# Performance work log

Hardware: AMD Instinct MI355X
Metric: run time of the kernel (lower is better)

## Reference

```python
import jax, jax.numpy as jnp
import numpy as np

NUM_HIGH = 3  # init arg num_high


def conv_gauss(img, kernel):
    # reflect pad 2 on H/W, then 5x5 depthwise conv (groups = C)
    img = jnp.pad(img, ((0, 0), (0, 0), (2, 2), (2, 2)), mode='reflect')
    C = img.shape[1]
    return jax.lax.conv_general_dilated(
        img, kernel, window_strides=(1, 1), padding='VALID',
        dimension_numbers=('NCHW', 'OIHW', 'NCHW'), feature_group_count=C)


def upsample(x, kernel):
    # zero-interleave in H and W (equivalent to the cat/view/permute chain),
    # then gaussian depthwise conv
    B, C, H, W = x.shape
    up = jnp.zeros((B, C, 2 * H, 2 * W), dtype=x.dtype).at[:, :, ::2, ::2].set(x)
    return conv_gauss(up, kernel)


def setup_inputs() -> dict:
    key = jax.random.key(0)
    k1, k2 = jax.random.split(key)
    img = jax.random.normal(k1, (16, 3, 512, 512), dtype=jnp.float32)
    kernel = jax.random.normal(k2, (3, 1, 5, 5), dtype=jnp.float32) * 0.04
    return {"img": img, "kernel": kernel}


def reference(img, kernel):
    # pyramid_decom: with even H/W at every level, up always matches current's
    # shape, so the bicubic-interpolate fallback branch is dead (as in torch).
    current = img
    pyr = []
    for _ in range(NUM_HIGH):
        filtered = conv_gauss(current, kernel)
        down = filtered[:, :, ::2, ::2]
        up = upsample(down, kernel)
        pyr.append(current - up)
        current = down
    pyr.append(current)
    return tuple(pyr)
```

## Files before the change

### kernel.cpp

```cpp
#include <hip/hip_runtime.h>


#define B_ 16
#define C_ 3
#define DX 64
#define EW 72
#define SDW 72

typedef float f4v __attribute__((ext_vector_type(4)));
typedef float f2v __attribute__((ext_vector_type(2)));

__device__ __forceinline__ int reflect101(int t, int n) {
    t = (t < 0) ? -t : t;
    return (t >= n) ? (2 * n - 2 - t) : t;
}

template<int LOG2HW, int DY, bool NTST>
__global__ __launch_bounds__(32 * DY, 8) void lap_level_t(
    const float* __restrict__ in, const float* __restrict__ kern,
    float* __restrict__ down, float* __restrict__ pyr)
{
    constexpr int H  = 1 << LOG2HW, W = H;
    constexpr int H2 = H >> 1,      W2 = W >> 1;
    constexpr int IH = 2 * DY + 7;

    __shared__ float sE[IH][EW];
    __shared__ float sO[IH][EW];
    __shared__ float sDn[DY + 2][SDW];

    const int bc  = blockIdx.z;
    const int c   = bc % C_;
    const int dx0 = blockIdx.x * DX;
    const int dy0 = blockIdx.y * DY;
    const int gx0 = 2 * dx0 - 4;
    const int gy0 = 2 * dy0 - 4;
    const int tid = threadIdx.x;

    float kk[25];
    {
        const float* kc = kern + c * 25;
        #pragma unroll
        for (int i = 0; i < 25; ++i) kk[i] = kc[i];
    }

    const float* src = in + (size_t)bc * H * W;

    {
        const int q  = tid & 31;
        const int gx = gx0 + 4 * q;
        const bool colOK = (gx >= 0) && (gx + 3 < W);
        const int rb = tid >> 5;
        const float* p0 = src + (size_t)reflect101(gy0 + rb,      H) * W;
        const float* p1 = src + (size_t)reflect101(gy0 + rb + DY, H) * W;
        const float* p2 = src + (size_t)reflect101(gy0 + ((rb + 2 * DY < IH) ? rb + 2 * DY : rb), H) * W;
        float4 v0, v1, v2;
        if (colOK) {
            v0 = *(const float4*)(p0 + gx);
            v1 = *(const float4*)(p1 + gx);
            v2 = *(const float4*)(p2 + gx);
        } else {
            const int c0 = reflect101(gx, W), c1 = reflect101(gx + 1, W),
                      c2 = reflect101(gx + 2, W), c3 = reflect101(gx + 3, W);
            v0 = make_float4(p0[c0], p0[c1], p0[c2], p0[c3]);
            v1 = make_float4(p1[c0], p1[c1], p1[c2], p1[c3]);
            v2 = make_float4(p2[c0], p2[c1], p2[c2], p2[c3]);
        }
        *(float2*)&sE[rb][2 * q]      = make_float2(v0.x, v0.z);
        *(float2*)&sO[rb][2 * q]      = make_float2(v0.y, v0.w);
        *(float2*)&sE[rb + DY][2 * q] = make_float2(v1.x, v1.z);
        *(float2*)&sO[rb + DY][2 * q] = make_float2(v1.y, v1.w);
        if (rb + 2 * DY < IH) {
            *(float2*)&sE[rb + 2 * DY][2 * q] = make_float2(v2.x, v2.z);
            *(float2*)&sO[rb + 2 * DY][2 * q] = make_float2(v2.y, v2.w);
        }
        if (tid < 4 * IH && (tid & 3) < 3) {
            const int r   = tid >> 2;
            const int q2  = 32 + (tid & 3);
            const int gx2 = gx0 + 4 * q2;
            const float* row = src + (size_t)reflect101(gy0 + r, H) * W;
            float4 v;
            if (gx2 >= 0 && gx2 + 3 < W) v = *(const float4*)(row + gx2);
            else v = make_float4(row[reflect101(gx2, W)], row[reflect101(gx2 + 1, W)],
                                 row[reflect101(gx2 + 2, W)], row[reflect101(gx2 + 3, W)]);
            *(float2*)&sE[r][2 * q2] = make_float2(v.x, v.z);
            *(float2*)&sO[r][2 * q2] = make_float2(v.y, v.w);
        }
    }
    __syncthreads();

    {
        constexpr int NDM = (DY + 2) * 16;
        if (tid < NDM + (DY + 2)) {
            int dr, m0;
            if (tid < NDM) { dr = tid >> 4; m0 = (tid & 15) << 2; }
            else           { dr = tid - NDM; m0 = 64; }
            float o0 = 0.f, o1 = 0.f, o2 = 0.f, o3 = 0.f;
            #pragma unroll
            for (int i = 0; i < 5; ++i) {
                const int r = 2 * dr + i;
                const float4 e0 = *(const float4*)&sE[r][m0];
                const float2 e1 = *(const float2*)&sE[r][m0 + 4];
                const float4 q0 = *(const float4*)&sO[r][m0];
                const float2 q1 = *(const float2*)&sO[r][m0 + 4];
                const float k0 = kk[5*i], k1 = kk[5*i+1], k2 = kk[5*i+2],
                            k3 = kk[5*i+3], k4 = kk[5*i+4];
                o0 += e0.x * k0 + q0.x * k1 + e0.y * k2 + q0.y * k3 + e0.z * k4;
                o1 += e0.y * k0 + q0.y * k1 + e0.z * k2 + q0.z * k3 + e0.w * k4;
                o2 += e0.z * k0 + q0.z * k1 + e0.w * k2 + q0.w * k3 + e1.x * k4;
                o3 += e0.w * k0 + q0.w * k1 + e1.x * k2 + q1.x * k3 + e1.y * k4;
            }
            *(f4v*)&sDn[dr][m0] = (f4v){o0, o1, o2, o3};
        }
    }
    __syncthreads();

    {
        const int pq  = tid & 31;
        const int pr  = tid >> 5;
        const int gdy = dy0 + pr;
        const int rows0 = (gdy == 0)      ? pr + 2 : pr;
        const int rows1 = pr + 1;
        const int rows2 = (gdy == H2 - 1) ? pr + 1 : pr + 2;
        const bool leftE  = (dx0 == 0 && pq == 0);
        const bool rightE = (dx0 + 2 * pq + 1 == W2 - 1);

        float uee_a = 0, ueo_a = 0, uoe_a = 0, uoo_a = 0;
        float uee_b = 0, ueo_b = 0, uoe_b = 0, uoo_b = 0;
        #pragma unroll
        for (int i = 0; i < 3; ++i) {
            const int rr = (i == 0) ? rows0 : (i == 1) ? rows1 : rows2;
            const float2 va = *(const float2*)&sDn[rr][2 * pq];
            const float2 vb = *(const float2*)&sDn[rr][2 * pq + 2];
            float aL = va.x, aC = va.y, aR = vb.x;
            float bL = va.y, bC = vb.x, bR = vb.y;
            if (leftE)  aL = aR;
            if (rightE) bR = bC;
            uee_a += aL * kk[10*i+0] + aC * kk[10*i+2] + aR * kk[10*i+4];
            ueo_a += aC * kk[10*i+1] + aR * kk[10*i+3];
            uee_b += bL * kk[10*i+0] + bC * kk[10*i+2] + bR * kk[10*i+4];
            ueo_b += bC * kk[10*i+1] + bR * kk[10*i+3];
            if (i) {
                uoe_a += aL * kk[10*i-5] + aC * kk[10*i-3] + aR * kk[10*i-1];
                uoo_a += aC * kk[10*i-4] + aR * kk[10*i-2];
                uoe_b += bL * kk[10*i-5] + bC * kk[10*i-3] + bR * kk[10*i-1];
                uoo_b += bC * kk[10*i-4] + bR * kk[10*i-2];
            }
            if (i == 1) {
                float* dp = down + (size_t)bc * H2 * W2 + (size_t)gdy * W2 + dx0 + 2 * pq;
                if constexpr (NTST) __builtin_nontemporal_store((f2v){aC, bC}, (f2v*)dp);
                else                *(float2*)dp = make_float2(aC, bC);
            }
        }

        const int ly = 2 * pr + 4;
        const int u  = 2 * pq + 2;
        const float2 e0 = *(const float2*)&sE[ly][u];
        const float2 q0 = *(const float2*)&sO[ly][u];
        const float2 e1 = *(const float2*)&sE[ly + 1][u];
        const float2 q1 = *(const float2*)&sO[ly + 1][u];

        float* py = pyr + (size_t)bc * H * W;
        const size_t base = (size_t)(2 * gdy) * W + (2 * dx0 + 4 * pq);
        const f4v o0 = {e0.x - uee_a, q0.x - ueo_a, e0.y - uee_b, q0.y - ueo_b};
        const f4v o1 = {e1.x - uoe_a, q1.x - uoo_a, e1.y - uoe_b, q1.y - uoo_b};
        __builtin_nontemporal_store(o0, (f4v*)(py + base));
        __builtin_nontemporal_store(o1, (f4v*)(py + base + W));
    }
}

__global__ __launch_bounds__(256) void down_kernel(
    const float* __restrict__ in, const float* __restrict__ kern,
    float* __restrict__ out, int H, int W)
{
    const int H2 = H >> 1, W2 = W >> 1;
    const int bc = blockIdx.z;
    const int c  = bc % C_;
    __shared__ float k[25];
    int tid = threadIdx.y * blockDim.x + threadIdx.x;
    if (tid < 25) k[tid] = kern[c * 25 + tid];
    __syncthreads();
    int x = blockIdx.x * blockDim.x + threadIdx.x;
    int y = blockIdx.y * blockDim.y + threadIdx.y;
    if (x >= W2 || y >= H2) return;
    const float* img = in + (size_t)bc * H * W;
    const int bx = 2 * x - 2, by = 2 * y - 2;
    float acc = 0.f;
    if (bx >= 0 && by >= 0 && bx + 4 < W && by + 4 < H) {
        const float* p = img + (size_t)by * W + bx;
        #pragma unroll
        for (int dy = 0; dy < 5; ++dy) {
            #pragma unroll
            for (int dx = 0; dx < 5; ++dx) acc += p[dx] * k[dy * 5 + dx];
            p += W;
        }
    } else {
        #pragma unroll
        for (int dy = 0; dy < 5; ++dy) {
            const float* row = img + (size_t)reflect101(by + dy, H) * W;
            #pragma unroll
            for (int dx = 0; dx < 5; ++dx) acc += row[reflect101(bx + dx, W)] * k[dy * 5 + dx];
        }
    }
    out[(size_t)bc * H2 * W2 + (size_t)y * W2 + x] = acc;
}

__global__ __launch_bounds__(256) void upsub_kernel(
    const float* __restrict__ cur, const float* __restrict__ kern,
    const float* __restrict__ down, float* __restrict__ pyr,
    int H2, int W2)
{
    const int H = H2 * 2, W = W2 * 2;
    const int bc = blockIdx.z;
    const int c  = bc % C_;
    __shared__ float k[25];
    int tid = threadIdx.y * blockDim.x + threadIdx.x;
    if (tid < 25) k[tid] = kern[c * 25 + tid];
    __syncthreads();
    int x2 = blockIdx.x * blockDim.x + threadIdx.x;
    int y2 = blockIdx.y * blockDim.y + threadIdx.y;
    if (x2 >= W2 || y2 >= H2) return;
    const float* dn = down + (size_t)bc * H2 * W2;
    const float* cu = cur  + (size_t)bc * H * W;
    float*       py = pyr  + (size_t)bc * H * W;
    const int xm = (x2 == 0)      ? 1      : x2 - 1;
    const int xp = (x2 == W2 - 1) ? W2 - 1 : x2 + 1;
    const int ym = (y2 == 0)      ? 1      : y2 - 1;
    const int yp = (y2 == H2 - 1) ? H2 - 1 : y2 + 1;
    float d[3][3];
    {
        const float* r0 = dn + (size_t)ym * W2;
        const float* r1 = dn + (size_t)y2 * W2;
        const float* r2 = dn + (size_t)yp * W2;
        d[0][0] = r0[xm]; d[0][1] = r0[x2]; d[0][2] = r0[xp];
        d[1][0] = r1[xm]; d[1][1] = r1[x2]; d[1][2] = r1[xp];
        d[2][0] = r2[xm]; d[2][1] = r2[x2]; d[2][2] = r2[xp];
    }
    float uee = 0.f, ueo = 0.f, uoe = 0.f, uoo = 0.f;
    #pragma unroll
    for (int i = 0; i < 3; ++i) {
        #pragma unroll
        for (int j = 0; j < 3; ++j) {
            const float v = d[i][j];
            uee += v * k[(2 * i) * 5 + 2 * j];
            if (j)      ueo += v * k[(2 * i) * 5 + 2 * j - 1];
            if (i)      uoe += v * k[(2 * i - 1) * 5 + 2 * j];
            if (i && j) uoo += v * k[(2 * i - 1) * 5 + 2 * j - 1];
        }
    }
    const int y = 2 * y2, x = 2 * x2;
    const float2 c0 = *(const float2*)(cu + (size_t)y       * W + x);
    const float2 c1 = *(const float2*)(cu + (size_t)(y + 1) * W + x);
    *(float2*)(py + (size_t)y       * W + x) = make_float2(c0.x - uee, c0.y - ueo);
    *(float2*)(py + (size_t)(y + 1) * W + x) = make_float2(c1.x - uoe, c1.y - uoo);
}

extern "C" void kernel_launch(void* const* d_in, const int* in_sizes, int n_in,
                              void* d_out, int out_size, void* d_ws, size_t ws_size,
                              hipStream_t stream) {
    const float* img  = (const float*)d_in[0];
    const float* kern = (const float*)d_in[1];
    float* out = (float*)d_out;

    const size_t n0 = (size_t)B_ * C_ * 512 * 512;
    const size_t n1 = (size_t)B_ * C_ * 256 * 256;
    const size_t n2 = (size_t)B_ * C_ * 128 * 128;

    float* pyr0  = out;
    float* pyr1  = out + n0;
    float* pyr2  = out + n0 + n1;
    float* down3 = out + n0 + n1 + n2;

    const int BC = B_ * C_;
    const size_t need = (n1 + n2) * sizeof(float);

    if (ws_size >= need) {
        float* down1 = (float*)d_ws;
        float* down2 = down1 + n1;
        lap_level_t<9, 16, false><<<dim3(256 / DX, 256 / 16, BC), 512, 0, stream>>>(img,   kern, down1, pyr0);
        lap_level_t<8, 16, false><<<dim3(128 / DX, 128 / 16, BC), 512, 0, stream>>>(down1, kern, down2, pyr1);
        lap_level_t<7,  8, true ><<<dim3( 64 / DX,  64 /  8, BC), 256, 0, stream>>>(down2, kern, down3, pyr2);
    } else {
        float* down1 = pyr1;
        float* down2 = pyr2;
        const dim3 blk(64, 4, 1);
        auto g2 = [&](int W2, int H2) { return dim3((W2 + 63) / 64, (H2 + 3) / 4, BC); };
        down_kernel <<<g2(256, 256), blk, 0, stream>>>(img, kern, down1, 512, 512);
        upsub_kernel<<<g2(256, 256), blk, 0, stream>>>(img, kern, down1, pyr0, 256, 256);
        down_kernel <<<g2(128, 128), blk, 0, stream>>>(down1, kern, down2, 256, 256);
        upsub_kernel<<<g2(128, 128), blk, 0, stream>>>(down1, kern, down2, pyr1, 128, 128);
        down_kernel <<<g2( 64,  64), blk, 0, stream>>>(down2, kern, down3, 128, 128);
        upsub_kernel<<<g2( 64,  64), blk, 0, stream>>>(down2, kern, down3, pyr2, 64, 64);
    }
}
```

Baseline: 45.78 us.

## Process multiple row tiles per block with register-prefetched next tile loads

```diff
diff --git a/kernel.cpp b/kernel.cpp
--- a/kernel.cpp
+++ b/kernel.cpp
@@ -15,8 +15,8 @@
     return (t >= n) ? (2 * n - 2 - t) : t;
 }
 
-template<int LOG2HW, int DY, bool NTST>
-__global__ __launch_bounds__(32 * DY, 8) void lap_level_t(
+template<int LOG2HW, int DY, int NT, bool NTST>
+__global__ __launch_bounds__(32 * DY, (NT == 1 ? 8 : 6)) void lap_level_t(
     const float* __restrict__ in, const float* __restrict__ kern,
     float* __restrict__ down, float* __restrict__ pyr)
 {
@@ -28,13 +28,13 @@
     __shared__ float sO[IH][EW];
     __shared__ float sDn[DY + 2][SDW];
 
-    const int bc  = blockIdx.z;
-    const int c   = bc % C_;
-    const int dx0 = blockIdx.x * DX;
-    const int dy0 = blockIdx.y * DY;
-    const int gx0 = 2 * dx0 - 4;
-    const int gy0 = 2 * dy0 - 4;
-    const int tid = threadIdx.x;
+    const int bc      = blockIdx.z;
+    const int c       = bc % C_;
+    const int dx0     = blockIdx.x * DX;
+    const int dy0base = blockIdx.y * (NT * DY);
+    const int gx0     = 2 * dx0 - 4;
+    const int gy0base = 2 * dy0base - 4;
+    const int tid     = threadIdx.x;
 
     float kk[25];
     {
@@ -45,126 +45,152 @@
 
     const float* src = in + (size_t)bc * H * W;
 
-    {
-        const int q  = tid & 31;
-        const int gx = gx0 + 4 * q;
-        const bool colOK = (gx >= 0) && (gx + 3 < W);
-        const int rb = tid >> 5;
-        const float* p0 = src + (size_t)reflect101(gy0 + rb,      H) * W;
-        const float* p1 = src + (size_t)reflect101(gy0 + rb + DY, H) * W;
-        const float* p2 = src + (size_t)reflect101(gy0 + ((rb + 2 * DY < IH) ? rb + 2 * DY : rb), H) * W;
-        float4 v0, v1, v2;
+    const int q  = tid & 31;
+    const int rb = tid >> 5;
+    const int gx = gx0 + 4 * q;
+    const bool colOK = (gx >= 0) && (gx + 3 < W);
+    int cx0 = 0, cx1 = 0, cx2 = 0, cx3 = 0;
+    if (!colOK) {
+        cx0 = reflect101(gx, W);     cx1 = reflect101(gx + 1, W);
+        cx2 = reflect101(gx + 2, W); cx3 = reflect101(gx + 3, W);
+    }
+    const bool sideOn = (tid < 4 * IH) && ((tid & 3) < 3);
+    const int rs  = tid >> 2;
+    const int q2  = 32 + (tid & 3);
+    const int gx2 = gx0 + 4 * q2;
+    const bool sideOK = (gx2 >= 0) && (gx2 + 3 < W);
+    int sx0 = 0, sx1 = 0, sx2 = 0, sx3 = 0;
+    if (sideOn && !sideOK) {
+        sx0 = reflect101(gx2, W);     sx1 = reflect101(gx2 + 1, W);
+        sx2 = reflect101(gx2 + 2, W); sx3 = reflect101(gx2 + 3, W);
+    }
+
+    float4 m0, m1, m2, sv;
+
+    auto LOADR = [&](int ty) {
+        const int gy0t = gy0base + 2 * DY * ty;
+        const float* p0 = src + (size_t)reflect101(gy0t + rb,      H) * W;
+        const float* p1 = src + (size_t)reflect101(gy0t + rb + DY, H) * W;
+        const float* p2 = src + (size_t)reflect101(gy0t + ((rb + 2 * DY < IH) ? rb + 2 * DY : rb), H) * W;
         if (colOK) {
-            v0 = *(const float4*)(p0 + gx);
-            v1 = *(const float4*)(p1 + gx);
-            v2 = *(const float4*)(p2 + gx);
+            m0 = *(const float4*)(p0 + gx);
+            m1 = *(const float4*)(p1 + gx);
+            m2 = *(const float4*)(p2 + gx);
         } else {
-            const int c0 = reflect101(gx, W), c1 = reflect101(gx + 1, W),
-                      c2 = reflect101(gx + 2, W), c3 = reflect101(gx + 3, W);
-            v0 = make_float4(p0[c0], p0[c1], p0[c2], p0[c3]);
-            v1 = make_float4(p1[c0], p1[c1], p1[c2], p1[c3]);
-            v2 = make_float4(p2[c0], p2[c1], p2[c2], p2[c3]);
-        }
-        *(float2*)&sE[rb][2 * q]      = make_float2(v0.x, v0.z);
-        *(float2*)&sO[rb][2 * q]      = make_float2(v0.y, v0.w);
-        *(float2*)&sE[rb + DY][2 * q] = make_float2(v1.x, v1.z);
-        *(float2*)&sO[rb + DY][2 * q] = make_float2(v1.y, v1.w);
+            m0 = make_float4(p0[cx0], p0[cx1], p0[cx2], p0[cx3]);
+            m1 = make_float4(p1[cx0], p1[cx1], p1[cx2], p1[cx3]);
+            m2 = make_float4(p2[cx0], p2[cx1], p2[cx2], p2[cx3]);
+        }
+        if (sideOn) {
+            const float* rowp = src + (size_t)reflect101(gy0t + rs, H) * W;
+            if (sideOK) sv = *(const float4*)(rowp + gx2);
+            else        sv = make_float4(rowp[sx0], rowp[sx1], rowp[sx2], rowp[sx3]);
+        }
+    };
+    auto DSW = [&]() {
+        *(float2*)&sE[rb][2 * q]      = make_float2(m0.x, m0.z);
+        *(float2*)&sO[rb][2 * q]      = make_float2(m0.y, m0.w);
+        *(float2*)&sE[rb + DY][2 * q] = make_float2(m1.x, m1.z);
+        *(float2*)&sO[rb + DY][2 * q] = make_float2(m1.y, m1.w);
         if (rb + 2 * DY < IH) {
-            *(float2*)&sE[rb + 2 * DY][2 * q] = make_float2(v2.x, v2.z);
-            *(float2*)&sO[rb + 2 * DY][2 * q] = make_float2(v2.y, v2.w);
-        }
-        if (tid < 4 * IH && (tid & 3) < 3) {
-            const int r   = tid >> 2;
-            const int q2  = 32 + (tid & 3);
-            const int gx2 = gx0 + 4 * q2;
-            const float* row = src + (size_t)reflect101(gy0 + r, H) * W;
-            float4 v;
-            if (gx2 >= 0 && gx2 + 3 < W) v = *(const float4*)(row + gx2);
-            else v = make_float4(row[reflect101(gx2, W)], row[reflect101(gx2 + 1, W)],
-                                 row[reflect101(gx2 + 2, W)], row[reflect101(gx2 + 3, W)]);
-            *(float2*)&sE[r][2 * q2] = make_float2(v.x, v.z);
-            *(float2*)&sO[r][2 * q2] = make_float2(v.y, v.w);
-        }
-    }
-    __syncthreads();
-
-    {
-        constexpr int NDM = (DY + 2) * 16;
-        if (tid < NDM + (DY + 2)) {
-            int dr, m0;
-            if (tid < NDM) { dr = tid >> 4; m0 = (tid & 15) << 2; }
-            else           { dr = tid - NDM; m0 = 64; }
-            float o0 = 0.f, o1 = 0.f, o2 = 0.f, o3 = 0.f;
+            *(float2*)&sE[rb + 2 * DY][2 * q] = make_float2(m2.x, m2.z);
+            *(float2*)&sO[rb + 2 * DY][2 * q] = make_float2(m2.y, m2.w);
+        }
+        if (sideOn) {
+            *(float2*)&sE[rs][2 * q2] = make_float2(sv.x, sv.z);
+            *(float2*)&sO[rs][2 * q2] = make_float2(sv.y, sv.w);
+        }
+    };
+
+    LOADR(0); DSW(); __syncthreads();
+
+    #pragma unroll
+    for (int ty = 0; ty < NT; ++ty) {
+        const int dy0 = dy0base + ty * DY;
+
+        if (ty + 1 < NT) LOADR(ty + 1);
+
+        {
+            constexpr int NDM = (DY + 2) * 16;
+            if (tid < NDM + (DY + 2)) {
+                int dr, m0i;
+                if (tid < NDM) { dr = tid >> 4; m0i = (tid & 15) << 2; }
+                else           { dr = tid - NDM; m0i = 64; }
+                float o0 = 0.f, o1 = 0.f, o2 = 0.f, o3 = 0.f;
+                #pragma unroll
+                for (int i = 0; i < 5; ++i) {
+                    const int r = 2 * dr + i;
+                    const float4 e0 = *(const float4*)&sE[r][m0i];
+                    const float2 e1 = *(const float2*)&sE[r][m0i + 4];
+                    const float4 q0 = *(const float4*)&sO[r][m0i];
+                    const float2 q1 = *(const float2*)&sO[r][m0i + 4];
+                    const float k0 = kk[5*i], k1 = kk[5*i+1], k2 = kk[5*i+2],
+                                k3 = kk[5*i+3], k4 = kk[5*i+4];
+                    o0 += e0.x * k0 + q0.x * k1 + e0.y * k2 + q0.y * k3 + e0.z * k4;
+                    o1 += e0.y * k0 + q0.y * k1 + e0.z * k2 + q0.z * k3 + e0.w * k4;
+                    o2 += e0.z * k0 + q0.z * k1 + e0.w * k2 + q0.w * k3 + e1.x * k4;
+                    o3 += e0.w * k0 + q0.w * k1 + e1.x * k2 + q1.x * k3 + e1.y * k4;
+                }
+                *(f4v*)&sDn[dr][m0i] = (f4v){o0, o1, o2, o3};
+            }
+        }
+        __syncthreads();
+
+        {
+            const int pq  = tid & 31;
+            const int pr  = tid >> 5;
+            const int gdy = dy0 + pr;
+            const int rows0 = (gdy == 0)      ? pr + 2 : pr;
+            const int rows1 = pr + 1;
+            const int rows2 = (gdy == H2 - 1) ? pr + 1 : pr + 2;
+            const bool leftE  = (dx0 == 0 && pq == 0);
+            const bool rightE = (dx0 + 2 * pq + 1 == W2 - 1);
+
+            float uee_a = 0, ueo_a = 0, uoe_a = 0, uoo_a = 0;
+            float uee_b = 0, ueo_b = 0, uoe_b = 0, uoo_b = 0;
             #pragma unroll
-            for (int i = 0; i < 5; ++i) {
-                const int r = 2 * dr + i;
-                const float4 e0 = *(const float4*)&sE[r][m0];
-                const float2 e1 = *(const float2*)&sE[r][m0 + 4];
-                const float4 q0 = *(const float4*)&sO[r][m0];
-                const float2 q1 = *(const float2*)&sO[r][m0 + 4];
-                const float k0 = kk[5*i], k1 = kk[5*i+1], k2 = kk[5*i+2],
-                            k3 = kk[5*i+3], k4 = kk[5*i+4];
-                o0 += e0.x * k0 + q0.x * k1 + e0.y * k2 + q0.y * k3 + e0.z * k4;
-                o1 += e0.y * k0 + q0.y * k1 + e0.z * k2 + q0.z * k3 + e0.w * k4;
-                o2 += e0.z * k0 + q0.z * k1 + e0.w * k2 + q0.w * k3 + e1.x * k4;
-                o3 += e0.w * k0 + q0.w * k1 + e1.x * k2 + q1.x * k3 + e1.y * k4;
+            for (int i = 0; i < 3; ++i) {
+                const int rr = (i == 0) ? rows0 : (i == 1) ? rows1 : rows2;
+                const float2 va = *(const float2*)&sDn[rr][2 * pq];
+                const float2 vb = *(const float2*)&sDn[rr][2 * pq + 2];
+                float aL = va.x, aC = va.y, aR = vb.x;
+                float bL = va.y, bC = vb.x, bR = vb.y;
+                if (leftE)  aL = aR;
+                if (rightE) bR = bC;
+                uee_a += aL * kk[10*i+0] + aC * kk[10*i+2] + aR * kk[10*i+4];
+                ueo_a += aC * kk[10*i+1] + aR * kk[10*i+3];
+                uee_b += bL * kk[10*i+0] + bC * kk[10*i+2] + bR * kk[10*i+4];
+                ueo_b += bC * kk[10*i+1] + bR * kk[10*i+3];
+                if (i) {
+                    uoe_a += aL * kk[10*i-5] + aC * kk[10*i-3] + aR * kk[10*i-1];
+                    uoo_a += aC * kk[10*i-4] + aR * kk[10*i-2];
+                    uoe_b += bL * kk[10*i-5] + bC * kk[10*i-3] + bR * kk[10*i-1];
+                    uoo_b += bC * kk[10*i-4] + bR * kk[10*i-2];
+                }
+                if (i == 1) {
+                    float* dp = down + (size_t)bc * H2 * W2 + (size_t)gdy * W2 + dx0 + 2 * pq;
+                    if constexpr (NTST) __builtin_nontemporal_store((f2v){aC, bC}, (f2v*)dp);
+                    else                *(float2*)dp = make_float2(aC, bC);
+                }
             }
-            *(f4v*)&sDn[dr][m0] = (f4v){o0, o1, o2, o3};
-        }
-    }
-    __syncthreads();
-
-    {
-        const int pq  = tid & 31;
-        const int pr  = tid >> 5;
-        const int gdy = dy0 + pr;
-        const int rows0 = (gdy == 0)      ? pr + 2 : pr;
-        const int rows1 = pr + 1;
-        const int rows2 = (gdy == H2 - 1) ? pr + 1 : pr + 2;
-        const bool leftE  = (dx0 == 0 && pq == 0);
-        const bool rightE = (dx0 + 2 * pq + 1 == W2 - 1);
-
-        float uee_a = 0, ueo_a = 0, uoe_a = 0, uoo_a = 0;
-        float uee_b = 0, ueo_b = 0, uoe_b = 0, uoo_b = 0;
-        #pragma unroll
-        for (int i = 0; i < 3; ++i) {
-            const int rr = (i == 0) ? rows0 : (i == 1) ? rows1 : rows2;
-            const float2 va = *(const float2*)&sDn[rr][2 * pq];
-            const float2 vb = *(const float2*)&sDn[rr][2 * pq + 2];
-            float aL = va.x, aC = va.y, aR = vb.x;
-            float bL = va.y, bC = vb.x, bR = vb.y;
-            if (leftE)  aL = aR;
-            if (rightE) bR = bC;
-            uee_a += aL * kk[10*i+0] + aC * kk[10*i+2] + aR * kk[10*i+4];
-            ueo_a += aC * kk[10*i+1] + aR * kk[10*i+3];
-            uee_b += bL * kk[10*i+0] + bC * kk[10*i+2] + bR * kk[10*i+4];
-            ueo_b += bC * kk[10*i+1] + bR * kk[10*i+3];
-            if (i) {
-                uoe_a += aL * kk[10*i-5] + aC * kk[10*i-3] + aR * kk[10*i-1];
-                uoo_a += aC * kk[10*i-4] + aR * kk[10*i-2];
-                uoe_b += bL * kk[10*i-5] + bC * kk[10*i-3] + bR * kk[10*i-1];
-                uoo_b += bC * kk[10*i-4] + bR * kk[10*i-2];
-            }
-            if (i == 1) {
-                float* dp = down + (size_t)bc * H2 * W2 + (size_t)gdy * W2 + dx0 + 2 * pq;
-                if constexpr (NTST) __builtin_nontemporal_store((f2v){aC, bC}, (f2v*)dp);
-                else                *(float2*)dp = make_float2(aC, bC);
-            }
-        }
-
-        const int ly = 2 * pr + 4;
-        const int u  = 2 * pq + 2;
-        const float2 e0 = *(const float2*)&sE[ly][u];
-        const float2 q0 = *(const float2*)&sO[ly][u];
-        const float2 e1 = *(const float2*)&sE[ly + 1][u];
-        const float2 q1 = *(const float2*)&sO[ly + 1][u];
-
-        float* py = pyr + (size_t)bc * H * W;
-        const size_t base = (size_t)(2 * gdy) * W + (2 * dx0 + 4 * pq);
-        const f4v o0 = {e0.x - uee_a, q0.x - ueo_a, e0.y - uee_b, q0.y - ueo_b};
-        const f4v o1 = {e1.x - uoe_a, q1.x - uoo_a, e1.y - uoe_b, q1.y - uoo_b};
-        __builtin_nontemporal_store(o0, (f4v*)(py + base));
-        __builtin_nontemporal_store(o1, (f4v*)(py + base + W));
+
+            const int ly = 2 * pr + 4;
+            const int u  = 2 * pq + 2;
+            const float2 e0 = *(const float2*)&sE[ly][u];
+            const float2 q0 = *(const float2*)&sO[ly][u];
+            const float2 e1 = *(const float2*)&sE[ly + 1][u];
+            const float2 q1 = *(const float2*)&sO[ly + 1][u];
+
+            float* py = pyr + (size_t)bc * H * W;
+            const size_t base = (size_t)(2 * gdy) * W + (2 * dx0 + 4 * pq);
+            const f4v o0 = {e0.x - uee_a, q0.x - ueo_a, e0.y - uee_b, q0.y - ueo_b};
+            const f4v o1 = {e1.x - uoe_a, q1.x - uoo_a, e1.y - uoe_b, q1.y - uoo_b};
+            __builtin_nontemporal_store(o0, (f4v*)(py + base));
+            __builtin_nontemporal_store(o1, (f4v*)(py + base + W));
+        }
+        __syncthreads();
+
+        if (ty + 1 < NT) { DSW(); __syncthreads(); }
     }
 }
 
@@ -276,9 +302,9 @@
     if (ws_size >= need) {
         float* down1 = (float*)d_ws;
         float* down2 = down1 + n1;
-        lap_level_t<9, 16, false><<<dim3(256 / DX, 256 / 16, BC), 512, 0, stream>>>(img,   kern, down1, pyr0);
-        lap_level_t<8, 16, false><<<dim3(128 / DX, 128 / 16, BC), 512, 0, stream>>>(down1, kern, down2, pyr1);
-        lap_level_t<7,  8, true ><<<dim3( 64 / DX,  64 /  8, BC), 256, 0, stream>>>(down2, kern, down3, pyr2);
+        lap_level_t<9, 16, 4, false><<<dim3(256 / DX, (256 / 16) / 4, BC), 512, 0, stream>>>(img,   kern, down1, pyr0);
+        lap_level_t<8, 16, 1, false><<<dim3(128 / DX, 128 / 16, BC), 512, 0, stream>>>(down1, kern, down2, pyr1);
+        lap_level_t<7,  8, 1, true ><<<dim3( 64 / DX,  64 /  8, BC), 256, 0, stream>>>(down2, kern, down3, pyr2);
     } else {
         float* down1 = pyr1;
         float* down2 = pyr2;
```

New measurement: 65.16 us. 1.42x slower.
